# Kernel optimization log

Measured on AMD Instinct MI355X. Metric: run time of the kernel, lower is better.

Reference implementation:

```python
import jax, jax.numpy as jnp
import numpy as np

B, S, D = 16, 2048, 128

def setup_inputs() -> dict:
    key = jax.random.key(0)
    kq, kk, kv = jax.random.split(key, 3)
    Q = jax.random.normal(kq, (B, S, D), dtype=jnp.float32)
    K = jax.random.normal(kk, (B, S, D), dtype=jnp.float32)
    V = jax.random.normal(kv, (B, S, D), dtype=jnp.float32)
    mask = jnp.ones((B, S), dtype=jnp.int32)  # key padding mask; 0 = masked out
    return {"Q": Q, "K": K, "V": V, "mask": mask}

def reference(Q, K, V, mask):
    scale = jnp.asarray(D ** 0.5, dtype=Q.dtype)
    # scores: [B, Sq, Sk]
    scores = jnp.einsum('bqd,bkd->bqk', Q, K) / scale
    neg_inf = jnp.asarray(float('-inf'), dtype=scores.dtype)
    # mask==0 -> -inf, broadcast over query dim: [B, 1, Sk]
    scores = jnp.where((mask == 0)[:, None, :], neg_inf, scores)
    attn = jax.nn.softmax(scores, axis=-1)
    out = jnp.einsum('bqk,bkd->bqd', attn, V)
    return (out, attn)
```

## Files before the change

kernel.cpp:

```cpp
#include <hip/hip_runtime.h>

#define BB 16
#define SS 2048
#define DD 128
#define SCALE 0.08838834764831845f

typedef __attribute__((ext_vector_type(8))) short bf16x8;
typedef __attribute__((ext_vector_type(4))) float f32x4;

__device__ __forceinline__ unsigned short f2bf(float f) {
    union { float f; unsigned int u; } v; v.f = f;
    unsigned int u = v.u;
    return (unsigned short)((u + 0x7fffu + ((u >> 16) & 1u)) >> 16);
}

__global__ __launch_bounds__(256) void cvt_bf16_kernel(const float* __restrict__ src,
                                                       unsigned short* __restrict__ dst) {
    int idx = (blockIdx.x * 256 + threadIdx.x) * 4;
    float4 f = *(const float4*)(src + idx);
    ushort4 o;
    o.x = f2bf(f.x); o.y = f2bf(f.y); o.z = f2bf(f.z); o.w = f2bf(f.w);
    *(ushort4*)(dst + idx) = o;
}

__global__ __launch_bounds__(256) void transpose_v_kernel(const float* __restrict__ v,
                                                          unsigned short* __restrict__ vt) {
    __shared__ unsigned short sT[64 * 132];
    int b = blockIdx.x >> 5;
    int s0 = (blockIdx.x & 31) * 64;
    int tid = threadIdx.x;
#pragma unroll
    for (int rnd = 0; rnd < 8; ++rnd) {
        int slot = rnd * 256 + tid;
        int row = slot >> 5;
        int c4 = (slot & 31) * 4;
        float4 f = *(const float4*)(v + (size_t)(b * SS + s0 + row) * DD + c4);
        unsigned short* p = &sT[row * 132 + c4];
        p[0] = f2bf(f.x); p[1] = f2bf(f.y); p[2] = f2bf(f.z); p[3] = f2bf(f.w);
    }
    __syncthreads();
#pragma unroll
    for (int rnd = 0; rnd < 4; ++rnd) {
        int slot = rnd * 256 + tid;
        int d = slot >> 3;
        int k8 = (slot & 7) * 8;
        __align__(16) unsigned short tmp[8];
#pragma unroll
        for (int e = 0; e < 8; ++e) tmp[e] = sT[(k8 + e) * 132 + d];
        *(ushort4*)(vt + (size_t)(b * DD + d) * SS + s0 + k8) = *(ushort4*)&tmp[0];
        *(ushort4*)(vt + (size_t)(b * DD + d) * SS + s0 + k8 + 4) = *(ushort4*)&tmp[4];
    }
}

__global__ __launch_bounds__(256) void attn_kernel(const unsigned short* __restrict__ Qb,
                                                   const unsigned short* __restrict__ Kb,
                                                   const unsigned short* __restrict__ Vt,
                                                   const int* __restrict__ mask,
                                                   float* __restrict__ outO,
                                                   float* __restrict__ outA) {
    __shared__ unsigned short sQ[64 * 136];
    __shared__ unsigned short sK[64 * 136];
    __shared__ unsigned short sV[128 * 72];
    __shared__ unsigned short sP[64 * 72];
    __shared__ float sLpart[2][64];
    __shared__ float sLinv[64];
    __shared__ float sMsk[64];

    int bi = blockIdx.x;
    int slot = bi >> 3;
    int b = (bi & 7) * 2 + (slot >> 5);
    int qt = slot & 31;

    int tid = threadIdx.x;
    int wave = tid >> 6, lane = tid & 63, lo = lane & 15, hi = lane >> 4;

    const unsigned short* Qbase = Qb + (size_t)(b * SS + qt * 64) * DD;
#pragma unroll
    for (int rnd = 0; rnd < 4; ++rnd) {
        int sl = rnd * 256 + tid;
        int row = sl >> 4, coff = (sl & 15) * 8;
        *(int4*)&sQ[row * 136 + coff] = *(const int4*)(Qbase + row * DD + coff);
    }
    if (tid < 64) { sLpart[0][tid] = 0.f; sLpart[1][tid] = 0.f; }

    const int r0 = (wave >> 1) * 32;
    const int c0 = (wave & 1) * 32;

    for (int kt = 0; kt < 32; ++kt) {
        __syncthreads();
        const unsigned short* Kbase = Kb + (size_t)(b * SS + kt * 64) * DD;
#pragma unroll
        for (int rnd = 0; rnd < 4; ++rnd) {
            int sl = rnd * 256 + tid;
            int row = sl >> 4, coff = (sl & 15) * 8;
            *(int4*)&sK[row * 136 + coff] = *(const int4*)(Kbase + row * DD + coff);
        }
        if (tid < 64) sMsk[tid] = mask[b * SS + kt * 64 + tid] ? 1.f : 0.f;
        __syncthreads();

        f32x4 acc[2][2];
#pragma unroll
        for (int ii = 0; ii < 2; ++ii)
#pragma unroll
            for (int jj = 0; jj < 2; ++jj) acc[ii][jj] = (f32x4){0.f, 0.f, 0.f, 0.f};
#pragma unroll
        for (int ks = 0; ks < 4; ++ks) {
            bf16x8 af[2], bf[2];
#pragma unroll
            for (int ii = 0; ii < 2; ++ii)
                af[ii] = *(const bf16x8*)&sQ[(r0 + ii * 16 + lo) * 136 + ks * 32 + hi * 8];
#pragma unroll
            for (int jj = 0; jj < 2; ++jj)
                bf[jj] = *(const bf16x8*)&sK[(c0 + jj * 16 + lo) * 136 + ks * 32 + hi * 8];
#pragma unroll
            for (int ii = 0; ii < 2; ++ii)
#pragma unroll
                for (int jj = 0; jj < 2; ++jj)
                    acc[ii][jj] = __builtin_amdgcn_mfma_f32_16x16x32_bf16(af[ii], bf[jj], acc[ii][jj], 0, 0, 0);
        }
        float m0 = sMsk[c0 + lo], m1 = sMsk[c0 + 16 + lo];
#pragma unroll
        for (int ii = 0; ii < 2; ++ii) {
#pragma unroll
            for (int r = 0; r < 4; ++r) {
                float v = __expf(acc[ii][0][r] * SCALE) * m0 + __expf(acc[ii][1][r] * SCALE) * m1;
                v += __shfl_xor(v, 1);
                v += __shfl_xor(v, 2);
                v += __shfl_xor(v, 4);
                v += __shfl_xor(v, 8);
                if (lo == 0) sLpart[wave & 1][r0 + ii * 16 + hi * 4 + r] += v;
            }
        }
    }
    __syncthreads();
    if (tid < 64) sLinv[tid] = 1.f / (sLpart[0][tid] + sLpart[1][tid]);

    f32x4 oacc[4][2];
#pragma unroll
    for (int mi = 0; mi < 4; ++mi)
#pragma unroll
        for (int tj = 0; tj < 2; ++tj) oacc[mi][tj] = (f32x4){0.f, 0.f, 0.f, 0.f};
    const int dv0 = wave * 32;

    for (int kt = 0; kt < 32; ++kt) {
        __syncthreads();
        const unsigned short* Kbase = Kb + (size_t)(b * SS + kt * 64) * DD;
#pragma unroll
        for (int rnd = 0; rnd < 4; ++rnd) {
            int sl = rnd * 256 + tid;
            int row = sl >> 4, coff = (sl & 15) * 8;
            *(int4*)&sK[row * 136 + coff] = *(const int4*)(Kbase + row * DD + coff);
        }
#pragma unroll
        for (int rnd = 0; rnd < 4; ++rnd) {
            int sl = rnd * 256 + tid;
            int row = sl >> 3, koff = (sl & 7) * 8;
            *(int4*)&sV[row * 72 + koff] =
                *(const int4*)(Vt + (size_t)(b * DD + row) * SS + kt * 64 + koff);
        }
        if (tid < 64) sMsk[tid] = mask[b * SS + kt * 64 + tid] ? 1.f : 0.f;
        __syncthreads();

        f32x4 acc[2][2];
#pragma unroll
        for (int ii = 0; ii < 2; ++ii)
#pragma unroll
            for (int jj = 0; jj < 2; ++jj) acc[ii][jj] = (f32x4){0.f, 0.f, 0.f, 0.f};
#pragma unroll
        for (int ks = 0; ks < 4; ++ks) {
            bf16x8 af[2], bf[2];
#pragma unroll
            for (int ii = 0; ii < 2; ++ii)
                af[ii] = *(const bf16x8*)&sQ[(r0 + ii * 16 + lo) * 136 + ks * 32 + hi * 8];
#pragma unroll
            for (int jj = 0; jj < 2; ++jj)
                bf[jj] = *(const bf16x8*)&sK[(c0 + jj * 16 + lo) * 136 + ks * 32 + hi * 8];
#pragma unroll
            for (int ii = 0; ii < 2; ++ii)
#pragma unroll
                for (int jj = 0; jj < 2; ++jj)
                    acc[ii][jj] = __builtin_amdgcn_mfma_f32_16x16x32_bf16(af[ii], bf[jj], acc[ii][jj], 0, 0, 0);
        }
        float m01[2] = {sMsk[c0 + lo], sMsk[c0 + 16 + lo]};
#pragma unroll
        for (int ii = 0; ii < 2; ++ii) {
#pragma unroll
            for (int jj = 0; jj < 2; ++jj) {
#pragma unroll
                for (int r = 0; r < 4; ++r) {
                    int row = r0 + ii * 16 + hi * 4 + r;
                    int col = c0 + jj * 16 + lo;
                    float p = __expf(acc[ii][jj][r] * SCALE) * m01[jj] * sLinv[row];
                    outA[(size_t)(b * SS + qt * 64 + row) * SS + kt * 64 + col] = p;
                    sP[row * 72 + col] = f2bf(p);
                }
            }
        }
        __syncthreads();

#pragma unroll
        for (int ks = 0; ks < 2; ++ks) {
            bf16x8 pa[4], vb[2];
#pragma unroll
            for (int mi = 0; mi < 4; ++mi)
                pa[mi] = *(const bf16x8*)&sP[(mi * 16 + lo) * 72 + ks * 32 + hi * 8];
#pragma unroll
            for (int tj = 0; tj < 2; ++tj)
                vb[tj] = *(const bf16x8*)&sV[(dv0 + tj * 16 + lo) * 72 + ks * 32 + hi * 8];
#pragma unroll
            for (int mi = 0; mi < 4; ++mi)
#pragma unroll
                for (int tj = 0; tj < 2; ++tj)
                    oacc[mi][tj] = __builtin_amdgcn_mfma_f32_16x16x32_bf16(pa[mi], vb[tj], oacc[mi][tj], 0, 0, 0);
        }
    }

#pragma unroll
    for (int mi = 0; mi < 4; ++mi) {
#pragma unroll
        for (int tj = 0; tj < 2; ++tj) {
#pragma unroll
            for (int r = 0; r < 4; ++r) {
                int row = mi * 16 + hi * 4 + r;
                int dv = dv0 + tj * 16 + lo;
                outO[(size_t)(b * SS + qt * 64 + row) * DD + dv] = oacc[mi][tj][r];
            }
        }
    }
}

extern "C" void kernel_launch(void* const* d_in, const int* in_sizes, int n_in,
                              void* d_out, int out_size, void* d_ws, size_t ws_size,
                              hipStream_t stream) {
    const float* Q = (const float*)d_in[0];
    const float* K = (const float*)d_in[1];
    const float* V = (const float*)d_in[2];
    const int* mask = (const int*)d_in[3];

    float* outO = (float*)d_out;
    float* outA = outO + (size_t)BB * SS * DD;

    unsigned short* Qb = (unsigned short*)d_ws;
    unsigned short* Kb = Qb + (size_t)BB * SS * DD;
    unsigned short* Vt = Kb + (size_t)BB * SS * DD;

    int nconv = (BB * SS * DD) / (256 * 4);
    cvt_bf16_kernel<<<nconv, 256, 0, stream>>>(Q, Qb);
    cvt_bf16_kernel<<<nconv, 256, 0, stream>>>(K, Kb);
    transpose_v_kernel<<<BB * (SS / 64), 256, 0, stream>>>(V, Vt);
    attn_kernel<<<BB * (SS / 64), 256, 0, stream>>>(Qb, Kb, Vt, mask, outO, outA);
}
```

Baseline: 455.8 us.

## Pipeline K/V tiles via async global-to-LDS loads with swizzled layout and transposed MFMA

Replaces synchronous register-staged K and V tile loads with global_load_lds async copies into double-buffered, XOR-swizzled LDS tiles, prefetching the next tile while the current one is computed. The S^T = K·Q^T product is computed with swapped operand roles so each lane holds four consecutive keys. This allows vectorized float4 stores of the attention matrix and output, and mask values are read straight from global memory. Row sums are kept in registers across the first pass instead of shuffle-reduced into shared memory every tile. The cost is more LDS, tighter synchronisation assumptions around async loads, and setprio hints.

```diff
diff --git a/kernel.cpp b/kernel.cpp
--- a/kernel.cpp
+++ b/kernel.cpp
@@ -12,6 +12,11 @@
     union { float f; unsigned int u; } v; v.f = f;
     unsigned int u = v.u;
     return (unsigned short)((u + 0x7fffu + ((u >> 16) & 1u)) >> 16);
+}
+
+__device__ __forceinline__ void gload16(const void* g, void* l) {
+    __builtin_amdgcn_global_load_lds((const __attribute__((address_space(1))) void*)g,
+                                     (__attribute__((address_space(3))) void*)l, 16, 0, 0);
 }
 
 __global__ __launch_bounds__(256) void cvt_bf16_kernel(const float* __restrict__ src,
@@ -58,13 +63,13 @@
                                                    const int* __restrict__ mask,
                                                    float* __restrict__ outO,
                                                    float* __restrict__ outA) {
+    __shared__ unsigned short sA[64 * 128];
+    __shared__ unsigned short sB[64 * 128];
+    __shared__ unsigned short sC[64 * 128];
     __shared__ unsigned short sQ[64 * 136];
-    __shared__ unsigned short sK[64 * 136];
-    __shared__ unsigned short sV[128 * 72];
     __shared__ unsigned short sP[64 * 72];
     __shared__ float sLpart[2][64];
     __shared__ float sLinv[64];
-    __shared__ float sMsk[64];
 
     int bi = blockIdx.x;
     int slot = bi >> 3;
@@ -73,6 +78,11 @@
 
     int tid = threadIdx.x;
     int wave = tid >> 6, lane = tid & 63, lo = lane & 15, hi = lane >> 4;
+    const int sw = lo & 7;
+
+    const int kq0 = (wave >> 1) * 32;
+    const int qq0 = (wave & 1) * 32;
+    const int dv0 = wave * 32;
 
     const unsigned short* Qbase = Qb + (size_t)(b * SS + qt * 64) * DD;
 #pragma unroll
@@ -81,123 +91,136 @@
         int row = sl >> 4, coff = (sl & 15) * 8;
         *(int4*)&sQ[row * 136 + coff] = *(const int4*)(Qbase + row * DD + coff);
     }
-    if (tid < 64) { sLpart[0][tid] = 0.f; sLpart[1][tid] = 0.f; }
-
-    const int r0 = (wave >> 1) * 32;
-    const int c0 = (wave & 1) * 32;
-
-    for (int kt = 0; kt < 32; ++kt) {
+
+    const char* KB = (const char*)(Kb + (size_t)b * SS * DD);
+    const char* VB = (const char*)(Vt + (size_t)b * DD * SS);
+    const int* maskB = mask + (size_t)b * SS;
+
+    const int RK = wave * 4 + (lane >> 4);
+    const unsigned CK = (unsigned)(RK * 256 + (((lane & 15) ^ (RK & 7)) << 4));
+    const unsigned CV = (unsigned)(wave * 32768 + (lane >> 3) * 4096 +
+                                   (((lane & 7) ^ (lane >> 3)) << 4));
+
+    auto ISSUE_K = [&](int kt, unsigned short* dst) {
+        const char* src = KB + (size_t)kt * 16384 + CK;
+        char* d = (char*)dst + wave * 1024;
+#pragma unroll
+        for (int i = 0; i < 4; ++i)
+            gload16(src + i * 4096, d + i * 4096);
+    };
+    auto ISSUE_V = [&](int kt, unsigned short* dst) {
+        const char* src = VB + (size_t)kt * 128 + CV;
+        char* d = (char*)dst + wave * 1024;
+#pragma unroll
+        for (int i = 0; i < 4; ++i)
+            gload16(src + (size_t)i * 131072, d + i * 4096);
+    };
+
+    auto QK = [&](const unsigned short* kb, f32x4 (&acc)[2][2]) {
+#pragma unroll
+        for (int ii = 0; ii < 2; ++ii)
+#pragma unroll
+            for (int jj = 0; jj < 2; ++jj) acc[ii][jj] = (f32x4){0.f, 0.f, 0.f, 0.f};
+        __builtin_amdgcn_s_setprio(1);
+#pragma unroll
+        for (int ks = 0; ks < 4; ++ks) {
+            bf16x8 af[2], bfr[2];
+#pragma unroll
+            for (int ii = 0; ii < 2; ++ii) {
+                int row = kq0 + ii * 16 + lo;
+                int ch = (ks * 4 + hi) ^ sw;
+                af[ii] = *(const bf16x8*)((const char*)kb + row * 256 + (ch << 4));
+            }
+#pragma unroll
+            for (int jj = 0; jj < 2; ++jj)
+                bfr[jj] = *(const bf16x8*)&sQ[(qq0 + jj * 16 + lo) * 136 + ks * 32 + hi * 8];
+#pragma unroll
+            for (int ii = 0; ii < 2; ++ii)
+#pragma unroll
+                for (int jj = 0; jj < 2; ++jj)
+                    acc[ii][jj] = __builtin_amdgcn_mfma_f32_16x16x32_bf16(af[ii], bfr[jj], acc[ii][jj], 0, 0, 0);
+        }
+        __builtin_amdgcn_s_setprio(0);
+    };
+
+    float lsum0 = 0.f, lsum1 = 0.f;
+
+    ISSUE_K(0, sA);
+#pragma unroll 1
+    for (int t = 0; t < 32; ++t) {
         __syncthreads();
-        const unsigned short* Kbase = Kb + (size_t)(b * SS + kt * 64) * DD;
-#pragma unroll
-        for (int rnd = 0; rnd < 4; ++rnd) {
-            int sl = rnd * 256 + tid;
-            int row = sl >> 4, coff = (sl & 15) * 8;
-            *(int4*)&sK[row * 136 + coff] = *(const int4*)(Kbase + row * DD + coff);
-        }
-        if (tid < 64) sMsk[tid] = mask[b * SS + kt * 64 + tid] ? 1.f : 0.f;
-        __syncthreads();
-
+        if (t < 31) ISSUE_K(t + 1, (t & 1) ? sA : sB);
         f32x4 acc[2][2];
-#pragma unroll
-        for (int ii = 0; ii < 2; ++ii)
-#pragma unroll
-            for (int jj = 0; jj < 2; ++jj) acc[ii][jj] = (f32x4){0.f, 0.f, 0.f, 0.f};
-#pragma unroll
-        for (int ks = 0; ks < 4; ++ks) {
-            bf16x8 af[2], bf[2];
-#pragma unroll
-            for (int ii = 0; ii < 2; ++ii)
-                af[ii] = *(const bf16x8*)&sQ[(r0 + ii * 16 + lo) * 136 + ks * 32 + hi * 8];
-#pragma unroll
-            for (int jj = 0; jj < 2; ++jj)
-                bf[jj] = *(const bf16x8*)&sK[(c0 + jj * 16 + lo) * 136 + ks * 32 + hi * 8];
-#pragma unroll
-            for (int ii = 0; ii < 2; ++ii)
-#pragma unroll
-                for (int jj = 0; jj < 2; ++jj)
-                    acc[ii][jj] = __builtin_amdgcn_mfma_f32_16x16x32_bf16(af[ii], bf[jj], acc[ii][jj], 0, 0, 0);
-        }
-        float m0 = sMsk[c0 + lo], m1 = sMsk[c0 + 16 + lo];
-#pragma unroll
-        for (int ii = 0; ii < 2; ++ii) {
-#pragma unroll
-            for (int r = 0; r < 4; ++r) {
-                float v = __expf(acc[ii][0][r] * SCALE) * m0 + __expf(acc[ii][1][r] * SCALE) * m1;
-                v += __shfl_xor(v, 1);
-                v += __shfl_xor(v, 2);
-                v += __shfl_xor(v, 4);
-                v += __shfl_xor(v, 8);
-                if (lo == 0) sLpart[wave & 1][r0 + ii * 16 + hi * 4 + r] += v;
-            }
+        QK((t & 1) ? sB : sA, acc);
+        int4 w0 = *(const int4*)(maskB + t * 64 + kq0 + hi * 4);
+        int4 w1 = *(const int4*)(maskB + t * 64 + kq0 + 16 + hi * 4);
+        float m0[4] = {w0.x ? 1.f : 0.f, w0.y ? 1.f : 0.f, w0.z ? 1.f : 0.f, w0.w ? 1.f : 0.f};
+        float m1[4] = {w1.x ? 1.f : 0.f, w1.y ? 1.f : 0.f, w1.z ? 1.f : 0.f, w1.w ? 1.f : 0.f};
+#pragma unroll
+        for (int r = 0; r < 4; ++r) {
+            lsum0 += __expf(acc[0][0][r] * SCALE) * m0[r] + __expf(acc[1][0][r] * SCALE) * m1[r];
+            lsum1 += __expf(acc[0][1][r] * SCALE) * m0[r] + __expf(acc[1][1][r] * SCALE) * m1[r];
+        }
+    }
+
+    {
+        float v0 = lsum0, v1 = lsum1;
+        v0 += __shfl_xor(v0, 16); v0 += __shfl_xor(v0, 32);
+        v1 += __shfl_xor(v1, 16); v1 += __shfl_xor(v1, 32);
+        if (lane < 16) {
+            sLpart[kq0 >> 5][qq0 + lane] = v0;
+            sLpart[kq0 >> 5][qq0 + 16 + lane] = v1;
         }
     }
     __syncthreads();
     if (tid < 64) sLinv[tid] = 1.f / (sLpart[0][tid] + sLpart[1][tid]);
-
-    f32x4 oacc[4][2];
-#pragma unroll
-    for (int mi = 0; mi < 4; ++mi)
-#pragma unroll
-        for (int tj = 0; tj < 2; ++tj) oacc[mi][tj] = (f32x4){0.f, 0.f, 0.f, 0.f};
-    const int dv0 = wave * 32;
-
-    for (int kt = 0; kt < 32; ++kt) {
+    __syncthreads();
+    const float linv0 = sLinv[qq0 + lo];
+    const float linv1 = sLinv[qq0 + 16 + lo];
+
+    f32x4 oacc[2][4];
+#pragma unroll
+    for (int tj = 0; tj < 2; ++tj)
+#pragma unroll
+        for (int mi = 0; mi < 4; ++mi) oacc[tj][mi] = (f32x4){0.f, 0.f, 0.f, 0.f};
+
+    float* Abase = outA + (size_t)(b * SS + qt * 64) * SS;
+
+    ISSUE_K(0, sA);
+    ISSUE_V(0, sB);
+#pragma unroll 1
+    for (int t = 0; t < 32; ++t) {
+        unsigned short* vcur = (t & 1) ? sC : sB;
         __syncthreads();
-        const unsigned short* Kbase = Kb + (size_t)(b * SS + kt * 64) * DD;
-#pragma unroll
-        for (int rnd = 0; rnd < 4; ++rnd) {
-            int sl = rnd * 256 + tid;
-            int row = sl >> 4, coff = (sl & 15) * 8;
-            *(int4*)&sK[row * 136 + coff] = *(const int4*)(Kbase + row * DD + coff);
-        }
-#pragma unroll
-        for (int rnd = 0; rnd < 4; ++rnd) {
-            int sl = rnd * 256 + tid;
-            int row = sl >> 3, koff = (sl & 7) * 8;
-            *(int4*)&sV[row * 72 + koff] =
-                *(const int4*)(Vt + (size_t)(b * DD + row) * SS + kt * 64 + koff);
-        }
-        if (tid < 64) sMsk[tid] = mask[b * SS + kt * 64 + tid] ? 1.f : 0.f;
+        if (t < 31) ISSUE_V(t + 1, (t & 1) ? sB : sC);
+        f32x4 acc[2][2];
+        QK(sA, acc);
+        int4 w0 = *(const int4*)(maskB + t * 64 + kq0 + hi * 4);
+        int4 w1 = *(const int4*)(maskB + t * 64 + kq0 + 16 + hi * 4);
+        float m0[4] = {w0.x ? 1.f : 0.f, w0.y ? 1.f : 0.f, w0.z ? 1.f : 0.f, w0.w ? 1.f : 0.f};
+        float m1[4] = {w1.x ? 1.f : 0.f, w1.y ? 1.f : 0.f, w1.z ? 1.f : 0.f, w1.w ? 1.f : 0.f};
+#pragma unroll
+        for (int jj = 0; jj < 2; ++jj) {
+            int q = qq0 + jj * 16 + lo;
+            float li = jj ? linv1 : linv0;
+#pragma unroll
+            for (int ii = 0; ii < 2; ++ii) {
+                f32x4 p;
+#pragma unroll
+                for (int r = 0; r < 4; ++r) {
+                    float mv = ii ? m1[r] : m0[r];
+                    p[r] = __expf(acc[ii][jj][r] * SCALE) * mv * li;
+                }
+                int kcol = kq0 + ii * 16 + hi * 4;
+                *(f32x4*)(Abase + (size_t)q * SS + t * 64 + kcol) = p;
+                ushort4 pb;
+                pb.x = f2bf(p[0]); pb.y = f2bf(p[1]); pb.z = f2bf(p[2]); pb.w = f2bf(p[3]);
+                *(ushort4*)&sP[q * 72 + kcol] = pb;
+            }
+        }
         __syncthreads();
-
-        f32x4 acc[2][2];
-#pragma unroll
-        for (int ii = 0; ii < 2; ++ii)
-#pragma unroll
-            for (int jj = 0; jj < 2; ++jj) acc[ii][jj] = (f32x4){0.f, 0.f, 0.f, 0.f};
-#pragma unroll
-        for (int ks = 0; ks < 4; ++ks) {
-            bf16x8 af[2], bf[2];
-#pragma unroll
-            for (int ii = 0; ii < 2; ++ii)
-                af[ii] = *(const bf16x8*)&sQ[(r0 + ii * 16 + lo) * 136 + ks * 32 + hi * 8];
-#pragma unroll
-            for (int jj = 0; jj < 2; ++jj)
-                bf[jj] = *(const bf16x8*)&sK[(c0 + jj * 16 + lo) * 136 + ks * 32 + hi * 8];
-#pragma unroll
-            for (int ii = 0; ii < 2; ++ii)
-#pragma unroll
-                for (int jj = 0; jj < 2; ++jj)
-                    acc[ii][jj] = __builtin_amdgcn_mfma_f32_16x16x32_bf16(af[ii], bf[jj], acc[ii][jj], 0, 0, 0);
-        }
-        float m01[2] = {sMsk[c0 + lo], sMsk[c0 + 16 + lo]};
-#pragma unroll
-        for (int ii = 0; ii < 2; ++ii) {
-#pragma unroll
-            for (int jj = 0; jj < 2; ++jj) {
-#pragma unroll
-                for (int r = 0; r < 4; ++r) {
-                    int row = r0 + ii * 16 + hi * 4 + r;
-                    int col = c0 + jj * 16 + lo;
-                    float p = __expf(acc[ii][jj][r] * SCALE) * m01[jj] * sLinv[row];
-                    outA[(size_t)(b * SS + qt * 64 + row) * SS + kt * 64 + col] = p;
-                    sP[row * 72 + col] = f2bf(p);
-                }
-            }
-        }
-        __syncthreads();
-
+        if (t < 31) ISSUE_K(t + 1, sA);
+        __builtin_amdgcn_s_setprio(1);
 #pragma unroll
         for (int ks = 0; ks < 2; ++ks) {
             bf16x8 pa[4], vb[2];
@@ -205,26 +228,28 @@
             for (int mi = 0; mi < 4; ++mi)
                 pa[mi] = *(const bf16x8*)&sP[(mi * 16 + lo) * 72 + ks * 32 + hi * 8];
 #pragma unroll
+            for (int tj = 0; tj < 2; ++tj) {
+                int rowv = dv0 + tj * 16 + lo;
+                int ch = (ks * 4 + hi) ^ sw;
+                vb[tj] = *(const bf16x8*)((const char*)vcur + rowv * 128 + (ch << 4));
+            }
+#pragma unroll
             for (int tj = 0; tj < 2; ++tj)
-                vb[tj] = *(const bf16x8*)&sV[(dv0 + tj * 16 + lo) * 72 + ks * 32 + hi * 8];
-#pragma unroll
-            for (int mi = 0; mi < 4; ++mi)
-#pragma unroll
-                for (int tj = 0; tj < 2; ++tj)
-                    oacc[mi][tj] = __builtin_amdgcn_mfma_f32_16x16x32_bf16(pa[mi], vb[tj], oacc[mi][tj], 0, 0, 0);
-        }
-    }
-
-#pragma unroll
-    for (int mi = 0; mi < 4; ++mi) {
-#pragma unroll
-        for (int tj = 0; tj < 2; ++tj) {
-#pragma unroll
-            for (int r = 0; r < 4; ++r) {
-                int row = mi * 16 + hi * 4 + r;
-                int dv = dv0 + tj * 16 + lo;
-                outO[(size_t)(b * SS + qt * 64 + row) * DD + dv] = oacc[mi][tj][r];
-            }
+#pragma unroll
+                for (int mi = 0; mi < 4; ++mi)
+                    oacc[tj][mi] = __builtin_amdgcn_mfma_f32_16x16x32_bf16(vb[tj], pa[mi], oacc[tj][mi], 0, 0, 0);
+        }
+        __builtin_amdgcn_s_setprio(0);
+    }
+
+    float* Obase = outO + (size_t)(b * SS + qt * 64) * DD;
+#pragma unroll
+    for (int tj = 0; tj < 2; ++tj) {
+#pragma unroll
+        for (int mi = 0; mi < 4; ++mi) {
+            int q = mi * 16 + lo;
+            int dv = dv0 + tj * 16 + hi * 4;
+            *(f32x4*)(Obase + (size_t)q * DD + dv) = oacc[tj][mi];
         }
     }
 }
```

Result: faster. 389.1 us (-14.6%).

## Rewrite attention core with register-resident 32x32 MFMA and split-K waves

Applied to the files above, without the earlier changes.

Replaces the LDS-staged 16x16 MFMA tiling with 32x32x16 MFMAs computing S^T per wave. Q fragments stay in registers, K and V fragments load straight from global memory, and P is exchanged between lanes with shuffles instead of going through shared memory. The waves split the key dimension in halves and reduce their O partials through LDS at the end. Attention output is written as float4 vector stores. This removes the per-tile __syncthreads and LDS staging, at the cost of more global-load traffic per wave (K read by two waves, no LDS reuse) and higher register pressure.

```diff
diff --git a/kernel.cpp b/kernel.cpp
--- a/kernel.cpp
+++ b/kernel.cpp
@@ -7,6 +7,7 @@
 
 typedef __attribute__((ext_vector_type(8))) short bf16x8;
 typedef __attribute__((ext_vector_type(4))) float f32x4;
+typedef __attribute__((ext_vector_type(16))) float f32x16;
 
 __device__ __forceinline__ unsigned short f2bf(float f) {
     union { float f; unsigned int u; } v; v.f = f;
@@ -58,13 +59,9 @@
                                                    const int* __restrict__ mask,
                                                    float* __restrict__ outO,
                                                    float* __restrict__ outA) {
-    __shared__ unsigned short sQ[64 * 136];
-    __shared__ unsigned short sK[64 * 136];
-    __shared__ unsigned short sV[128 * 72];
-    __shared__ unsigned short sP[64 * 72];
+    __shared__ float sO[64 * 132];
     __shared__ float sLpart[2][64];
     __shared__ float sLinv[64];
-    __shared__ float sMsk[64];
 
     int bi = blockIdx.x;
     int slot = bi >> 3;
@@ -72,160 +69,158 @@
     int qt = slot & 31;
 
     int tid = threadIdx.x;
-    int wave = tid >> 6, lane = tid & 63, lo = lane & 15, hi = lane >> 4;
-
-    const unsigned short* Qbase = Qb + (size_t)(b * SS + qt * 64) * DD;
-#pragma unroll
-    for (int rnd = 0; rnd < 4; ++rnd) {
-        int sl = rnd * 256 + tid;
-        int row = sl >> 4, coff = (sl & 15) * 8;
-        *(int4*)&sQ[row * 136 + coff] = *(const int4*)(Qbase + row * DD + coff);
-    }
-    if (tid < 64) { sLpart[0][tid] = 0.f; sLpart[1][tid] = 0.f; }
-
-    const int r0 = (wave >> 1) * 32;
-    const int c0 = (wave & 1) * 32;
-
-    for (int kt = 0; kt < 32; ++kt) {
-        __syncthreads();
-        const unsigned short* Kbase = Kb + (size_t)(b * SS + kt * 64) * DD;
-#pragma unroll
-        for (int rnd = 0; rnd < 4; ++rnd) {
-            int sl = rnd * 256 + tid;
-            int row = sl >> 4, coff = (sl & 15) * 8;
-            *(int4*)&sK[row * 136 + coff] = *(const int4*)(Kbase + row * DD + coff);
-        }
-        if (tid < 64) sMsk[tid] = mask[b * SS + kt * 64 + tid] ? 1.f : 0.f;
-        __syncthreads();
-
-        f32x4 acc[2][2];
-#pragma unroll
-        for (int ii = 0; ii < 2; ++ii)
-#pragma unroll
-            for (int jj = 0; jj < 2; ++jj) acc[ii][jj] = (f32x4){0.f, 0.f, 0.f, 0.f};
-#pragma unroll
-        for (int ks = 0; ks < 4; ++ks) {
-            bf16x8 af[2], bf[2];
-#pragma unroll
-            for (int ii = 0; ii < 2; ++ii)
-                af[ii] = *(const bf16x8*)&sQ[(r0 + ii * 16 + lo) * 136 + ks * 32 + hi * 8];
-#pragma unroll
-            for (int jj = 0; jj < 2; ++jj)
-                bf[jj] = *(const bf16x8*)&sK[(c0 + jj * 16 + lo) * 136 + ks * 32 + hi * 8];
-#pragma unroll
-            for (int ii = 0; ii < 2; ++ii)
-#pragma unroll
-                for (int jj = 0; jj < 2; ++jj)
-                    acc[ii][jj] = __builtin_amdgcn_mfma_f32_16x16x32_bf16(af[ii], bf[jj], acc[ii][jj], 0, 0, 0);
-        }
-        float m0 = sMsk[c0 + lo], m1 = sMsk[c0 + 16 + lo];
-#pragma unroll
-        for (int ii = 0; ii < 2; ++ii) {
-#pragma unroll
-            for (int r = 0; r < 4; ++r) {
-                float v = __expf(acc[ii][0][r] * SCALE) * m0 + __expf(acc[ii][1][r] * SCALE) * m1;
-                v += __shfl_xor(v, 1);
-                v += __shfl_xor(v, 2);
-                v += __shfl_xor(v, 4);
-                v += __shfl_xor(v, 8);
-                if (lo == 0) sLpart[wave & 1][r0 + ii * 16 + hi * 4 + r] += v;
+    int wave = tid >> 6, lane = tid & 63;
+    const int q5 = lane & 31;
+    const int h = lane >> 5;
+
+    const int kq0 = (wave >> 1) * 32;
+    const int qq0 = (wave & 1) * 32;
+
+    const unsigned short* Qlane = Qb + (size_t)(b * SS + qt * 64 + qq0 + q5) * DD + h * 8;
+    bf16x8 qf[8];
+#pragma unroll
+    for (int ks = 0; ks < 8; ++ks) qf[ks] = *(const bf16x8*)(Qlane + ks * 16);
+
+    const unsigned short* Klane = Kb + (size_t)b * SS * DD + (size_t)(kq0 + q5) * DD + h * 8;
+    const unsigned short* Vlane = Vt + (size_t)b * DD * SS + (size_t)q5 * SS + kq0 + h * 8;
+    const int* mlane = mask + (size_t)b * SS + kq0 + 4 * h;
+
+    float lsum = 0.f;
+#pragma unroll 1
+    for (int t = 0; t < 32; ++t) {
+        bf16x8 af[8];
+#pragma unroll
+        for (int ks = 0; ks < 8; ++ks)
+            af[ks] = *(const bf16x8*)(Klane + t * 8192 + ks * 16);
+        int4 mm[4];
+#pragma unroll
+        for (int g = 0; g < 4; ++g)
+            mm[g] = *(const int4*)(mlane + t * 64 + 8 * g);
+        f32x16 acc;
+#pragma unroll
+        for (int i = 0; i < 16; ++i) acc[i] = 0.f;
+        __builtin_amdgcn_s_setprio(1);
+#pragma unroll
+        for (int ks = 0; ks < 8; ++ks)
+            acc = __builtin_amdgcn_mfma_f32_32x32x16_bf16(af[ks], qf[ks], acc, 0, 0, 0);
+        __builtin_amdgcn_s_setprio(0);
+#pragma unroll
+        for (int g = 0; g < 4; ++g) {
+            float mv0 = mm[g].x ? 1.f : 0.f, mv1 = mm[g].y ? 1.f : 0.f;
+            float mv2 = mm[g].z ? 1.f : 0.f, mv3 = mm[g].w ? 1.f : 0.f;
+            lsum += __expf(acc[4 * g + 0] * SCALE) * mv0 + __expf(acc[4 * g + 1] * SCALE) * mv1 +
+                    __expf(acc[4 * g + 2] * SCALE) * mv2 + __expf(acc[4 * g + 3] * SCALE) * mv3;
+        }
+    }
+    lsum += __shfl_xor(lsum, 32);
+    if (lane < 32) sLpart[kq0 >> 5][qq0 + q5] = lsum;
+    __syncthreads();
+    if (tid < 64) sLinv[tid] = 1.f / (sLpart[0][tid] + sLpart[1][tid]);
+    __syncthreads();
+    const float linv = sLinv[qq0 + q5];
+
+    f32x16 oacc[4];
+#pragma unroll
+    for (int dvt = 0; dvt < 4; ++dvt)
+#pragma unroll
+        for (int i = 0; i < 16; ++i) oacc[dvt][i] = 0.f;
+
+    float* Abase = outA + (size_t)(b * SS + qt * 64 + qq0 + q5) * SS + kq0 + 4 * h;
+
+#pragma unroll 1
+    for (int t = 0; t < 32; ++t) {
+        bf16x8 af[8];
+#pragma unroll
+        for (int ks = 0; ks < 8; ++ks)
+            af[ks] = *(const bf16x8*)(Klane + t * 8192 + ks * 16);
+        bf16x8 vf[4][2];
+#pragma unroll
+        for (int dvt = 0; dvt < 4; ++dvt)
+#pragma unroll
+            for (int c = 0; c < 2; ++c)
+                vf[dvt][c] = *(const bf16x8*)(Vlane + (size_t)dvt * 32 * SS + t * 64 + c * 16);
+        int4 mm[4];
+#pragma unroll
+        for (int g = 0; g < 4; ++g)
+            mm[g] = *(const int4*)(mlane + t * 64 + 8 * g);
+
+        f32x16 acc;
+#pragma unroll
+        for (int i = 0; i < 16; ++i) acc[i] = 0.f;
+        __builtin_amdgcn_s_setprio(1);
+#pragma unroll
+        for (int ks = 0; ks < 8; ++ks)
+            acc = __builtin_amdgcn_mfma_f32_32x32x16_bf16(af[ks], qf[ks], acc, 0, 0, 0);
+        __builtin_amdgcn_s_setprio(0);
+
+        float p[16];
+#pragma unroll
+        for (int g = 0; g < 4; ++g) {
+            float mv0 = mm[g].x ? 1.f : 0.f, mv1 = mm[g].y ? 1.f : 0.f;
+            float mv2 = mm[g].z ? 1.f : 0.f, mv3 = mm[g].w ? 1.f : 0.f;
+            p[4 * g + 0] = __expf(acc[4 * g + 0] * SCALE) * mv0 * linv;
+            p[4 * g + 1] = __expf(acc[4 * g + 1] * SCALE) * mv1 * linv;
+            p[4 * g + 2] = __expf(acc[4 * g + 2] * SCALE) * mv2 * linv;
+            p[4 * g + 3] = __expf(acc[4 * g + 3] * SCALE) * mv3 * linv;
+        }
+#pragma unroll
+        for (int g = 0; g < 4; ++g) {
+            f32x4 st = {p[4 * g], p[4 * g + 1], p[4 * g + 2], p[4 * g + 3]};
+            *(f32x4*)(Abase + t * 64 + 8 * g) = st;
+        }
+        unsigned pw[4][2];
+#pragma unroll
+        for (int g = 0; g < 4; ++g) {
+            pw[g][0] = (unsigned)f2bf(p[4 * g]) | ((unsigned)f2bf(p[4 * g + 1]) << 16);
+            pw[g][1] = (unsigned)f2bf(p[4 * g + 2]) | ((unsigned)f2bf(p[4 * g + 3]) << 16);
+        }
+        bf16x8 pfrag[2];
+#pragma unroll
+        for (int c = 0; c < 2; ++c) {
+            unsigned s0 = h ? pw[2 * c][0] : pw[2 * c + 1][0];
+            unsigned s1 = h ? pw[2 * c][1] : pw[2 * c + 1][1];
+            unsigned r0 = (unsigned)__shfl_xor((int)s0, 32);
+            unsigned r1 = (unsigned)__shfl_xor((int)s1, 32);
+            union { unsigned u[4]; bf16x8 v; } pf;
+            pf.u[0] = h ? r0 : pw[2 * c][0];
+            pf.u[1] = h ? r1 : pw[2 * c][1];
+            pf.u[2] = h ? pw[2 * c + 1][0] : r0;
+            pf.u[3] = h ? pw[2 * c + 1][1] : r1;
+            pfrag[c] = pf.v;
+        }
+        __builtin_amdgcn_s_setprio(1);
+#pragma unroll
+        for (int dvt = 0; dvt < 4; ++dvt)
+#pragma unroll
+            for (int c = 0; c < 2; ++c)
+                oacc[dvt] = __builtin_amdgcn_mfma_f32_32x32x16_bf16(vf[dvt][c], pfrag[c], oacc[dvt], 0, 0, 0);
+        __builtin_amdgcn_s_setprio(0);
+    }
+
+    __syncthreads();
+    if (wave >= 2) {
+#pragma unroll
+        for (int dvt = 0; dvt < 4; ++dvt)
+#pragma unroll
+            for (int g = 0; g < 4; ++g) {
+                f32x4 v = {oacc[dvt][4 * g], oacc[dvt][4 * g + 1],
+                           oacc[dvt][4 * g + 2], oacc[dvt][4 * g + 3]};
+                *(f32x4*)&sO[(qq0 + q5) * 132 + dvt * 32 + 8 * g + 4 * h] = v;
             }
-        }
-    }
-    __syncthreads();
-    if (tid < 64) sLinv[tid] = 1.f / (sLpart[0][tid] + sLpart[1][tid]);
-
-    f32x4 oacc[4][2];
-#pragma unroll
-    for (int mi = 0; mi < 4; ++mi)
-#pragma unroll
-        for (int tj = 0; tj < 2; ++tj) oacc[mi][tj] = (f32x4){0.f, 0.f, 0.f, 0.f};
-    const int dv0 = wave * 32;
-
-    for (int kt = 0; kt < 32; ++kt) {
-        __syncthreads();
-        const unsigned short* Kbase = Kb + (size_t)(b * SS + kt * 64) * DD;
-#pragma unroll
-        for (int rnd = 0; rnd < 4; ++rnd) {
-            int sl = rnd * 256 + tid;
-            int row = sl >> 4, coff = (sl & 15) * 8;
-            *(int4*)&sK[row * 136 + coff] = *(const int4*)(Kbase + row * DD + coff);
-        }
-#pragma unroll
-        for (int rnd = 0; rnd < 4; ++rnd) {
-            int sl = rnd * 256 + tid;
-            int row = sl >> 3, koff = (sl & 7) * 8;
-            *(int4*)&sV[row * 72 + koff] =
-                *(const int4*)(Vt + (size_t)(b * DD + row) * SS + kt * 64 + koff);
-        }
-        if (tid < 64) sMsk[tid] = mask[b * SS + kt * 64 + tid] ? 1.f : 0.f;
-        __syncthreads();
-
-        f32x4 acc[2][2];
-#pragma unroll
-        for (int ii = 0; ii < 2; ++ii)
-#pragma unroll
-            for (int jj = 0; jj < 2; ++jj) acc[ii][jj] = (f32x4){0.f, 0.f, 0.f, 0.f};
-#pragma unroll
-        for (int ks = 0; ks < 4; ++ks) {
-            bf16x8 af[2], bf[2];
-#pragma unroll
-            for (int ii = 0; ii < 2; ++ii)
-                af[ii] = *(const bf16x8*)&sQ[(r0 + ii * 16 + lo) * 136 + ks * 32 + hi * 8];
-#pragma unroll
-            for (int jj = 0; jj < 2; ++jj)
-                bf[jj] = *(const bf16x8*)&sK[(c0 + jj * 16 + lo) * 136 + ks * 32 + hi * 8];
-#pragma unroll
-            for (int ii = 0; ii < 2; ++ii)
-#pragma unroll
-                for (int jj = 0; jj < 2; ++jj)
-                    acc[ii][jj] = __builtin_amdgcn_mfma_f32_16x16x32_bf16(af[ii], bf[jj], acc[ii][jj], 0, 0, 0);
-        }
-        float m01[2] = {sMsk[c0 + lo], sMsk[c0 + 16 + lo]};
-#pragma unroll
-        for (int ii = 0; ii < 2; ++ii) {
-#pragma unroll
-            for (int jj = 0; jj < 2; ++jj) {
-#pragma unroll
-                for (int r = 0; r < 4; ++r) {
-                    int row = r0 + ii * 16 + hi * 4 + r;
-                    int col = c0 + jj * 16 + lo;
-                    float p = __expf(acc[ii][jj][r] * SCALE) * m01[jj] * sLinv[row];
-                    outA[(size_t)(b * SS + qt * 64 + row) * SS + kt * 64 + col] = p;
-                    sP[row * 72 + col] = f2bf(p);
-                }
+    }
+    __syncthreads();
+    if (wave < 2) {
+        float* Obase = outO + (size_t)(b * SS + qt * 64 + qq0 + q5) * DD;
+#pragma unroll
+        for (int dvt = 0; dvt < 4; ++dvt)
+#pragma unroll
+            for (int g = 0; g < 4; ++g) {
+                int dv = dvt * 32 + 8 * g + 4 * h;
+                f32x4 o = *(const f32x4*)&sO[(qq0 + q5) * 132 + dv];
+                f32x4 v = {oacc[dvt][4 * g] + o[0], oacc[dvt][4 * g + 1] + o[1],
+                           oacc[dvt][4 * g + 2] + o[2], oacc[dvt][4 * g + 3] + o[3]};
+                *(f32x4*)(Obase + dv) = v;
             }
-        }
-        __syncthreads();
-
-#pragma unroll
-        for (int ks = 0; ks < 2; ++ks) {
-            bf16x8 pa[4], vb[2];
-#pragma unroll
-            for (int mi = 0; mi < 4; ++mi)
-                pa[mi] = *(const bf16x8*)&sP[(mi * 16 + lo) * 72 + ks * 32 + hi * 8];
-#pragma unroll
-            for (int tj = 0; tj < 2; ++tj)
-                vb[tj] = *(const bf16x8*)&sV[(dv0 + tj * 16 + lo) * 72 + ks * 32 + hi * 8];
-#pragma unroll
-            for (int mi = 0; mi < 4; ++mi)
-#pragma unroll
-                for (int tj = 0; tj < 2; ++tj)
-                    oacc[mi][tj] = __builtin_amdgcn_mfma_f32_16x16x32_bf16(pa[mi], vb[tj], oacc[mi][tj], 0, 0, 0);
-        }
-    }
-
-#pragma unroll
-    for (int mi = 0; mi < 4; ++mi) {
-#pragma unroll
-        for (int tj = 0; tj < 2; ++tj) {
-#pragma unroll
-            for (int r = 0; r < 4; ++r) {
-                int row = mi * 16 + hi * 4 + r;
-                int dv = dv0 + tj * 16 + lo;
-                outO[(size_t)(b * SS + qt * 64 + row) * DD + dv] = oacc[mi][tj][r];
-            }
-        }
     }
 }
 
```

After: 501.0 us. 9.9% more time.
